# Optimization experiments

Hardware: AMD Instinct MI355X
Metric: run time of the kernel (lower is better)

Reference implementation:

```python
import jax, jax.numpy as jnp
import numpy as np

NALGOS = 64
NTASKS = 256
T = 4096  # len(lx)


def setup_inputs() -> dict:
    key = jax.random.key(0)
    ks = jax.random.split(key, 6)
    return {
        "lx": jax.random.randint(ks[0], (T,), 0, NTASKS),
        # task_matrix ~ U(-1, 1), as in the torch init
        "task_matrix": jax.random.uniform(ks[1], (NTASKS, NTASKS), jnp.float32) * 2.0 - 1.0,
        # task difficulty ~ U(0, 1); keep away from 0 to avoid division blowup
        "task_difficulty": jax.random.uniform(ks[2], (NTASKS,), jnp.float32, 0.05, 1.0),
        "alg_efficiency": 0.5 + 0.02 * jax.random.normal(ks[3], (NALGOS,), jnp.float32),
        "alg_memory_horizon": 0.5 + 0.1 * jax.random.normal(ks[4], (NALGOS,), jnp.float32),
        "alg_experience_boost": 0.5 + 0.02 * jax.random.normal(ks[5], (NALGOS,), jnp.float32),
    }


def reference(lx, task_matrix, task_difficulty, alg_efficiency,
              alg_memory_horizon, alg_experience_boost):
    # Faithful translation of IdealLearner.performance.
    # Original triple loop reads result[algo,task2,ind] and sig[algo,task,ind]
    # (previous timestep only) and writes index ind+1, so each timestep is
    # vectorizable over (algo, task2); only the time axis is a true recurrence.
    A = alg_efficiency.shape[0]
    N = task_matrix.shape[0]
    eff = alg_efficiency[:, None]        # (A,1)
    mem = alg_memory_horizon[:, None]    # (A,1)
    boost = alg_experience_boost[:, None]  # (A,1)
    diff = task_difficulty[None, :]      # (1,N) ; task_difficulty_scale == 1

    def step(carry, task):
        res_prev, sig_prev = carry              # each (A, N)
        tm = task_matrix[task][None, :]         # (1, N) row for current task
        sp = sig_prev[:, task][:, None]         # (A, 1) prior perf on current task
        res = res_prev * mem + tm * eff + tm * sp * boost
        sig = 2.0 * jax.nn.sigmoid(res / diff) - 1.0
        return (res, sig), sig

    z = jnp.zeros((A, N), task_matrix.dtype)
    _, ys = jax.lax.scan(step, (z, z), lx)      # ys: (T, A, N)
    # prepend the zero initial state -> (A, N, T+1), matching the torch output
    return jnp.concatenate([z[:, :, None], jnp.transpose(ys, (1, 2, 0))], axis=-1)
```

## Files before the change

kernel.cpp:

```cpp
#include <hip/hip_runtime.h>
#include <hip/hip_bf16.h>

#define NALGOS 64
#define NTASKS 256
#define TSTEPS 4096
#define CHUNK  256
#define NCHUNK (TSTEPS / CHUNK)
#define SUB    32
#define TP     257
#define LOG2E  1.44269504f

__global__ __launch_bounds__(64) void driver_kernel(
    const int* __restrict__ lx, const float* __restrict__ tmat,
    const float* __restrict__ diff, const float* __restrict__ eff_v,
    const float* __restrict__ mem_v, const float* __restrict__ boost_v,
    float* __restrict__ g_arr, float* __restrict__ ckpt) {
  __shared__ int    lx_s[TSTEPS + 16];
  __shared__ float  c_s[NTASKS];
  __shared__ float4 ctab[TSTEPS + 8];
  __shared__ int    itab[TSTEPS + 8];

  const int a = blockIdx.x;
  const int l = threadIdx.x;
  const float eff   = eff_v[a];
  const float mem   = mem_v[a];
  const float boost = boost_v[a];
  const float e0 = eff - boost;
  const float b2 = 2.0f * boost;
  const float m2 = mem * mem;

#pragma unroll 8
  for (int k = 0; k < TSTEPS / 64; ++k) lx_s[k * 64 + l] = lx[k * 64 + l];
  if (l < 16) lx_s[TSTEPS + l] = 0;
#pragma unroll
  for (int k = 0; k < NTASKS / 64; ++k) {
    float dk = diff[k * 64 + l];
    c_s[k * 64 + l] = -LOG2E / dk;
  }
  __syncthreads();

#pragma unroll 4
  for (int k = 0; k < TSTEPS / 64; ++k) {
    int i  = k * 64 + l;
    int t1 = lx_s[i + 1];
    float q  = tmat[lx_s[i] * NTASKS + t1];
    float q2 = (i >= 1) ? tmat[lx_s[i - 1] * NTASKS + t1]
                        : 0.f;
    float cp = c_s[t1];
    float4 e;
    e.x = b2 * cp * q;
    e.y = b2 * cp * mem * q2;
    e.z = e0 * cp * (q + mem * q2);
    e.w = cp * m2;
    ctab[i] = e;
    itab[i] = lx_s[i + 3] | (lx_s[i + 8] << 16);
  }
  if (l < 8) {
    ctab[TSTEPS + l] = make_float4(0.f, 0.f, 0.f, 0.f);
    itab[TSTEPS + l] = 0;
  }
  __syncthreads();

  const float4* rows = (const float4*)tmat;
  float* gout = g_arr + (size_t)a * TSTEPS;
  float* ck   = ckpt  + (size_t)a * NCHUNK * NTASKS;

  float r0 = 0.f, r1 = 0.f, r2 = 0.f, r3 = 0.f;
  float u = 2.0f;
  float keep_g = 0.f;

  float4 ctr[4];
  int    itr[4];
  float4 tmr[8];
#pragma unroll
  for (int k = 0; k < 4; ++k) { ctr[k] = ctab[k]; itr[k] = itab[k]; }
#pragma unroll
  for (int k = 0; k < 8; ++k) tmr[k] = rows[lx_s[k] * 64 + l];
  float A    = ctr[0].z;
  float base = ctr[1].z;

  for (int grp = 0; grp < TSTEPS / 64; ++grp) {
#pragma unroll 1
    for (int k32 = 0; k32 < 2; ++k32) {
      const float4* cb = ctab + grp * 64 + k32 * 32;
      const int*    ib = itab + grp * 64 + k32 * 32;
      const int kb = k32 * 32;
#pragma unroll
      for (int kk = 0; kk < 32; ++kk) {
        const int k = kb + kk;
        const float4 ct0 = ctr[k & 3];
        const float4 ct1 = ctr[(k + 1) & 3];
        const float4 ct2 = ctr[(k + 2) & 3];
        const float4 tm  = tmr[k & 7];
        const int    it  = itr[k & 3];

        float w   = __builtin_amdgcn_rcpf(u);
        float arg = fmaf(ct0.x, w, A);
        float ev  = __builtin_amdgcn_exp2f(arg);
        u = 1.0f + ev;

        float gt = fmaf(b2, w, e0);
        A = fmaf(ct1.y, w, base);

        keep_g = (k == l) ? gt : keep_g;

        r0 = fmaf(r0, mem, tm.x * gt);
        r1 = fmaf(r1, mem, tm.y * gt);
        r2 = fmaf(r2, mem, tm.z * gt);
        r3 = fmaf(r3, mem, tm.w * gt);

        const int sw   = __builtin_amdgcn_readfirstlane(it);
        const int j    = sw & 0xff;
        const int lane = j >> 2;
        float h01  = (j & 1) ? r1 : r0;
        float h23  = (j & 1) ? r3 : r2;
        float hsel = (j & 2) ? h23 : h01;
        float bro = __uint_as_float(
            __builtin_amdgcn_readlane(__float_as_uint(hsel), lane));
        base = fmaf(ct2.w, bro, ct2.z);

        ctr[k & 3] = cb[kk + 4];
        itr[k & 3] = ib[kk + 4];
        const int nrow = (sw >> 16) & 0xff;
        tmr[k & 7] = rows[nrow * 64 + l];
      }
    }
    gout[grp * 64 + l] = keep_g;
    if ((grp & 3) == 3 && grp != 63) {
      float4 s; s.x = r0; s.y = r1; s.z = r2; s.w = r3;
      ((float4*)(ck + ((grp + 1) >> 2) * NTASKS))[l] = s;
    }
  }
}

__global__ __launch_bounds__(256) void expand_kernel(
    const int* __restrict__ lx, const float* __restrict__ tmat,
    const float* __restrict__ diff, const float* __restrict__ mem_v,
    const float* __restrict__ g_arr, const float* __restrict__ ckpt,
    float* __restrict__ out) {
  __shared__ float tile[SUB * TP];
  __shared__ int   lx_c[CHUNK];
  __shared__ float g_c[CHUNK];

  const int id = blockIdx.x;
  const int c  = (id >> 3) & 15;
  const int a  = (id & 7) + 8 * (id >> 7);
  const int n  = threadIdx.x;

  const float mem = mem_v[a];
  const float cn  = -LOG2E / diff[n];
  float res = (c == 0) ? 0.f : ckpt[((size_t)a * NCHUNK + c) * NTASKS + n];

  const int t0 = c * CHUNK;
  lx_c[n] = lx[t0 + n];
  g_c[n]  = g_arr[(size_t)a * TSTEPS + t0 + n];
  __syncthreads();

  if (c == 0) out[((size_t)a * NTASKS + n) * (TSTEPS + 1)] = 0.f;

  const int tq   = threadIdx.x & 7;
  const int rloc = threadIdx.x >> 3;

  for (int tb = 0; tb < CHUNK; tb += SUB) {
#pragma unroll 8
    for (int ts = 0; ts < SUB; ++ts) {
      int   task = lx_c[tb + ts];
      float g    = g_c[tb + ts];
      float tm   = tmat[task * NTASKS + n];
      res = fmaf(res, mem, tm * g);
      float w = __builtin_amdgcn_rcpf(
          1.0f + __builtin_amdgcn_exp2f(cn * res));
      tile[ts * TP + n] = fmaf(2.0f, w, -1.0f);
    }
    __syncthreads();
    for (int rr = 0; rr < NTASKS; rr += 32) {
      const int row = rr + rloc;
      float v0 = tile[(4 * tq + 0) * TP + row];
      float v1 = tile[(4 * tq + 1) * TP + row];
      float v2 = tile[(4 * tq + 2) * TP + row];
      float v3 = tile[(4 * tq + 3) * TP + row];
      float4 v = make_float4(v0, v1, v2, v3);
      float* dst = &out[((size_t)a * NTASKS + row) * (TSTEPS + 1) +
                        t0 + tb + 4 * tq + 1];
      __builtin_memcpy(dst, &v, 16);
    }
    __syncthreads();
  }
}

extern "C" void kernel_launch(void* const* d_in, const int* in_sizes, int n_in,
                              void* d_out, int out_size, void* d_ws, size_t ws_size,
                              hipStream_t stream) {
  const int*   lx    = (const int*)d_in[0];
  const float* tmat  = (const float*)d_in[1];
  const float* diff  = (const float*)d_in[2];
  const float* eff   = (const float*)d_in[3];
  const float* mem   = (const float*)d_in[4];
  const float* boost = (const float*)d_in[5];
  float* out = (float*)d_out;

  float* g_arr = (float*)d_ws;
  float* ckpt  = g_arr + (size_t)NALGOS * TSTEPS;

  driver_kernel<<<NALGOS, 64, 0, stream>>>(lx, tmat, diff, eff, mem, boost,
                                           g_arr, ckpt);
  expand_kernel<<<dim3(NCHUNK * NALGOS), 256, 0, stream>>>(
      lx, tmat, diff, mem, g_arr, ckpt, out);
}
```

Baseline: 655.7 us.

## Restructure expand kernel into 64-thread blocks with per-row tile and aligned vector stores

Splits the expand kernel into 64-thread blocks, each covering 64 tasks of one algorithm over a 256-step chunk. Each thread computes its whole chunk row into a shared tile, prefetching task-matrix values 16 steps ahead in registers. It then writes its own output row with alignment-adjusted float4 stores instead of the old transpose pattern. This removes the intermediate barriers and the strided transposed reads, but each thread now writes one long contiguous row. The shared tile grows to about 64KB, which may limit occupancy. The driver kernel's prefetch register index changes from k&7 to kk&7; this is equivalent because kb is a multiple of 32.

```diff
diff --git a/kernel.cpp b/kernel.cpp
--- a/kernel.cpp
+++ b/kernel.cpp
@@ -6,8 +6,7 @@
 #define TSTEPS 4096
 #define CHUNK  256
 #define NCHUNK (TSTEPS / CHUNK)
-#define SUB    32
-#define TP     257
+#define TPT    257
 #define LOG2E  1.44269504f
 
 __global__ __launch_bounds__(64) void driver_kernel(
@@ -44,8 +43,7 @@
     int i  = k * 64 + l;
     int t1 = lx_s[i + 1];
     float q  = tmat[lx_s[i] * NTASKS + t1];
-    float q2 = (i >= 1) ? tmat[lx_s[i - 1] * NTASKS + t1]
-                        : 0.f;
+    float q2 = (i >= 1) ? tmat[lx_s[i - 1] * NTASKS + t1] : 0.f;
     float cp = c_s[t1];
     float4 e;
     e.x = b2 * cp * q;
@@ -122,7 +120,7 @@
         ctr[k & 3] = cb[kk + 4];
         itr[k & 3] = ib[kk + 4];
         const int nrow = (sw >> 16) & 0xff;
-        tmr[k & 7] = rows[nrow * 64 + l];
+        tmr[kk & 7] = rows[nrow * 64 + l];
       }
     }
     gout[grp * 64 + l] = keep_g;
@@ -133,59 +131,74 @@
   }
 }
 
-__global__ __launch_bounds__(256) void expand_kernel(
+__global__ __launch_bounds__(64) void expand_kernel(
     const int* __restrict__ lx, const float* __restrict__ tmat,
     const float* __restrict__ diff, const float* __restrict__ mem_v,
     const float* __restrict__ g_arr, const float* __restrict__ ckpt,
     float* __restrict__ out) {
-  __shared__ float tile[SUB * TP];
-  __shared__ int   lx_c[CHUNK];
+  __shared__ float tile[64 * TPT];
+  __shared__ int   lx_c[CHUNK + 16];
   __shared__ float g_c[CHUNK];
 
   const int id = blockIdx.x;
-  const int c  = (id >> 3) & 15;
-  const int a  = (id & 7) + 8 * (id >> 7);
-  const int n  = threadIdx.x;
+  const int c  = id >> 8;
+  const int r8 = id & 255;
+  const int a  = r8 >> 2;
+  const int ng = r8 & 3;
+  const int l  = threadIdx.x;
+  const int n  = ng * 64 + l;
 
   const float mem = mem_v[a];
   const float cn  = -LOG2E / diff[n];
+  const int t0 = c * CHUNK;
+
+#pragma unroll
+  for (int i = 0; i < 4; ++i) {
+    lx_c[i * 64 + l] = lx[t0 + i * 64 + l];
+    g_c[i * 64 + l]  = g_arr[(size_t)a * TSTEPS + t0 + i * 64 + l];
+  }
+  if (l < 16) lx_c[CHUNK + l] = 0;
+  __syncthreads();
+
   float res = (c == 0) ? 0.f : ckpt[((size_t)a * NCHUNK + c) * NTASKS + n];
 
-  const int t0 = c * CHUNK;
-  lx_c[n] = lx[t0 + n];
-  g_c[n]  = g_arr[(size_t)a * TSTEPS + t0 + n];
-  __syncthreads();
-
-  if (c == 0) out[((size_t)a * NTASKS + n) * (TSTEPS + 1)] = 0.f;
-
-  const int tq   = threadIdx.x & 7;
-  const int rloc = threadIdx.x >> 3;
-
-  for (int tb = 0; tb < CHUNK; tb += SUB) {
-#pragma unroll 8
-    for (int ts = 0; ts < SUB; ++ts) {
-      int   task = lx_c[tb + ts];
-      float g    = g_c[tb + ts];
-      float tm   = tmat[task * NTASKS + n];
-      res = fmaf(res, mem, tm * g);
-      float w = __builtin_amdgcn_rcpf(
-          1.0f + __builtin_amdgcn_exp2f(cn * res));
-      tile[ts * TP + n] = fmaf(2.0f, w, -1.0f);
-    }
-    __syncthreads();
-    for (int rr = 0; rr < NTASKS; rr += 32) {
-      const int row = rr + rloc;
-      float v0 = tile[(4 * tq + 0) * TP + row];
-      float v1 = tile[(4 * tq + 1) * TP + row];
-      float v2 = tile[(4 * tq + 2) * TP + row];
-      float v3 = tile[(4 * tq + 3) * TP + row];
-      float4 v = make_float4(v0, v1, v2, v3);
-      float* dst = &out[((size_t)a * NTASKS + row) * (TSTEPS + 1) +
-                        t0 + tb + 4 * tq + 1];
-      __builtin_memcpy(dst, &v, 16);
-    }
-    __syncthreads();
-  }
+  {
+    float w = __builtin_amdgcn_rcpf(1.0f + __builtin_amdgcn_exp2f(cn * res));
+    tile[l * TPT + 0] = fmaf(2.0f, w, -1.0f);
+  }
+
+  float tmr[16];
+#pragma unroll
+  for (int i = 0; i < 16; ++i) tmr[i] = tmat[lx_c[i] * NTASKS + n];
+
+#pragma unroll 16
+  for (int s = 0; s < CHUNK; ++s) {
+    float tm = tmr[s & 15];
+    res = fmaf(res, mem, tm * g_c[s]);
+    float w = __builtin_amdgcn_rcpf(1.0f + __builtin_amdgcn_exp2f(cn * res));
+    tile[l * TPT + s + 1] = fmaf(2.0f, w, -1.0f);
+    tmr[s & 15] = tmat[lx_c[s + 16] * NTASKS + n];
+  }
+  __syncthreads();
+
+  const float* trow = &tile[l * TPT];
+  float* orow = out + ((size_t)a * NTASKS + n) * (size_t)(TSTEPS + 1) + t0;
+  const int j0 = (-n) & 3;
+#pragma unroll
+  for (int h = 0; h < 3; ++h)
+    if (h < j0) orow[h] = trow[h];
+  const int nb = (CHUNK - j0) >> 2;
+  for (int b = 0; b < nb; ++b) {
+    const int col = j0 + 4 * b;
+    float4 v = make_float4(trow[col], trow[col + 1], trow[col + 2], trow[col + 3]);
+    *reinterpret_cast<float4*>(orow + col) = v;
+  }
+#pragma unroll
+  for (int t2 = 0; t2 < 3; ++t2) {
+    const int col = j0 + 4 * nb + t2;
+    if (col < CHUNK) orow[col] = trow[col];
+  }
+  if (c == NCHUNK - 1) orow[CHUNK] = trow[CHUNK];
 }
 
 extern "C" void kernel_launch(void* const* d_in, const int* in_sizes, int n_in,
@@ -204,6 +217,6 @@
 
   driver_kernel<<<NALGOS, 64, 0, stream>>>(lx, tmat, diff, eff, mem, boost,
                                            g_arr, ckpt);
-  expand_kernel<<<dim3(NCHUNK * NALGOS), 256, 0, stream>>>(
+  expand_kernel<<<dim3(NCHUNK * NALGOS * 4), 64, 0, stream>>>(
       lx, tmat, diff, mem, g_arr, ckpt, out);
 }
```

After: 877.2 us. +33.8%, slower.
